# Kernel tuning notes

Hardware: AMD Instinct MI355X
Metric: run time of the kernel (lower is better)

The kernel has to match this reference:

```python
import jax, jax.numpy as jnp
import numpy as np

B, N, D_MODEL, H = 4, 2048, 1024, 16  # batch, seq, model dim, heads


def setup_inputs() -> dict:
    key = jax.random.key(0)
    k1, k2, k3 = jax.random.split(key, 3)
    x = jax.random.normal(k1, (B, N, D_MODEL), dtype=jnp.float32)
    # nn.Linear weights: [out_features, in_features]; scaled for stability
    Wqkv = jax.random.normal(k2, (3 * D_MODEL, D_MODEL), dtype=jnp.float32) * 0.02
    bqkv = jnp.zeros((3 * D_MODEL,), dtype=jnp.float32)
    Wo = jax.random.normal(k3, (D_MODEL, D_MODEL), dtype=jnp.float32) * 0.02
    bo = jnp.zeros((D_MODEL,), dtype=jnp.float32)
    return {"x": x, "Wqkv": Wqkv, "bqkv": bqkv, "Wo": Wo, "bo": bo}


def reference(x, Wqkv, bqkv, Wo, bo):
    b, n, _ = x.shape
    qkv = x @ Wqkv.T + bqkv                      # [b, n, 3*d_model]
    # rearrange 'b n (h d) -> b h n d' with h heads, then chunk into q,k,v
    qkv = qkv.reshape(b, n, H, -1).transpose(0, 2, 1, 3)  # [b, h, n, 3*dh]
    q, k, v = jnp.split(qkv, 3, axis=-1)          # each [b, h, n, dh]
    scale = k.shape[-1] ** 0.5
    scores = jnp.einsum('bhqd,bhkd->bhqk', q, k) / scale
    attn = jax.nn.softmax(scores, axis=-1)
    out = jnp.einsum('bhqk,bhkd->bhqd', attn, v)  # [b, h, n, dh]
    out = out.transpose(0, 2, 1, 3).reshape(b, n, -1)  # 'b h n d -> b n (h d)'
    return out @ Wo.T + bo
```

## Files before the change

### kernel.cpp

```cpp
#include <hip/hip_runtime.h>
#include <hip/hip_bf16.h>

using bf16 = __hip_bfloat16;
typedef __attribute__((ext_vector_type(8))) __bf16 bf16x8;
typedef __attribute__((ext_vector_type(4))) float f32x4;
typedef __attribute__((ext_vector_type(16))) float f32x16;
typedef __attribute__((ext_vector_type(4))) unsigned u32x4;

#define MFMA16(a, b, c) __builtin_amdgcn_mfma_f32_16x16x32_bf16((a), (b), (c), 0, 0, 0)
#define MFMA32(a, b, c) __builtin_amdgcn_mfma_f32_32x32x16_bf16((a), (b), (c), 0, 0, 0)

static __device__ __forceinline__ void gload_lds16(const bf16* g, bf16* l) {
    __builtin_amdgcn_global_load_lds(
        (__attribute__((address_space(1))) void*)(bf16*)(g),
        (__attribute__((address_space(3))) void*)(l), 16, 0, 0);
}

static __device__ __forceinline__ unsigned cvtpk(float lo, float hi) {
    unsigned r;
    asm("v_cvt_pk_bf16_f32 %0, %1, %2" : "=v"(r) : "v"(lo), "v"(hi));
    return r;
}

__global__ void cvt_f32_bf16(const float* __restrict__ in, bf16* __restrict__ out, int n4) {
    int i = blockIdx.x * 256 + threadIdx.x;
    if (i >= n4) return;
    float4 v = ((const float4*)in)[i];
    bf16 t[4];
    t[0] = __float2bfloat16(v.x);
    t[1] = __float2bfloat16(v.y);
    t[2] = __float2bfloat16(v.z);
    t[3] = __float2bfloat16(v.w);
    *(uint2*)(out + 4l * i) = *(uint2*)t;
}

__global__ void gemm_qkv(const bf16* __restrict__ A, const bf16* __restrict__ B,
                         const float* __restrict__ bias,
                         bf16* __restrict__ Qo, bf16* __restrict__ Ko, bf16* __restrict__ Vt) {
    const int K = 1024;
    __shared__ bf16 Alds[128 * 32];
    __shared__ bf16 Blds[128 * 32];
    int t = threadIdx.x;
    int lane = t & 63;
    int wave = t >> 6;
    int wm = wave >> 1, wn = wave & 1;
    int r = lane & 15, q = lane >> 4;
    long m0 = (long)blockIdx.y * 128;
    long n0 = (long)blockIdx.x * 128;
    const bf16* Ab = A + m0 * K;
    const bf16* Bb = B + n0 * K;

    f32x4 acc[4][4] = {};

    int srow = t >> 2;
    int scol = (t & 3) << 3;

    for (int k0 = 0; k0 < K; k0 += 32) {
        __syncthreads();
        gload_lds16(Ab + (long)srow * K + k0 + scol, Alds + t * 8);
        gload_lds16(Ab + (long)(srow + 64) * K + k0 + scol, Alds + 2048 + t * 8);
        gload_lds16(Bb + (long)srow * K + k0 + scol, Blds + t * 8);
        gload_lds16(Bb + (long)(srow + 64) * K + k0 + scol, Blds + 2048 + t * 8);
        __syncthreads();

        bf16x8 af[4], bfv[4];
#pragma unroll
        for (int mi = 0; mi < 4; mi++)
            af[mi] = *(const bf16x8*)(Alds + (wm * 64 + mi * 16 + r) * 32 + q * 8);
#pragma unroll
        for (int ni = 0; ni < 4; ni++)
            bfv[ni] = *(const bf16x8*)(Blds + (wn * 64 + ni * 16 + r) * 32 + q * 8);
#pragma unroll
        for (int mi = 0; mi < 4; mi++)
#pragma unroll
            for (int ni = 0; ni < 4; ni++)
                acc[mi][ni] = MFMA16(af[mi], bfv[ni], acc[mi][ni]);
    }

#pragma unroll
    for (int ni = 0; ni < 4; ni++) {
        int n = (int)n0 + wn * 64 + ni * 16 + r;
        float bn = bias[n];
        int h = n / 192;
        int rem = n % 192;
        int part = rem >> 6;
        int d = rem & 63;
#pragma unroll
        for (int mi = 0; mi < 4; mi++) {
#pragma unroll
            for (int rr = 0; rr < 4; rr++) {
                int m = (int)m0 + wm * 64 + mi * 16 + q * 4 + rr;
                int b = m >> 11;
                int row = m & 2047;
                long bh = b * 16 + h;
                bf16 bv = __float2bfloat16(acc[mi][ni][rr] + bn);
                if (part == 0)      Qo[(bh * 2048 + row) * 64 + d] = bv;
                else if (part == 1) Ko[(bh * 2048 + row) * 64 + d] = bv;
                else                Vt[(bh * 64 + d) * 2048 + row] = bv;
            }
        }
    }
}


#define PACK8(S, OFF, OUTV) { \
    unsigned A0 = cvtpk(S[OFF+0], S[OFF+1]); \
    unsigned B0 = cvtpk(S[OFF+4], S[OFF+5]); \
    unsigned A1 = cvtpk(S[OFF+2], S[OFF+3]); \
    unsigned B1 = cvtpk(S[OFF+6], S[OFF+7]); \
    asm("v_permlane32_swap_b32 %0, %1" : "+v"(A0), "+v"(B0)); \
    asm("v_permlane32_swap_b32 %0, %1" : "+v"(A1), "+v"(B1)); \
    u32x4 W; W.x = A0; W.y = A1; W.z = B0; W.w = B1; \
    OUTV = __builtin_bit_cast(bf16x8, W); }

#define COMPUTE(KB, VB) do { \
    f32x16 sA = {}, sB = {}; \
    __builtin_amdgcn_s_setprio(1); \
    { \
        bf16x8 kA, kB; \
        kA = *(const bf16x8*)(KB + (0 * 64 + lane) * 8); \
        kB = *(const bf16x8*)(KB + (256 + 0 * 64 + lane) * 8); \
        sA = MFMA32(kA, qf0, sA);  sB = MFMA32(kB, qf0, sB); \
        kA = *(const bf16x8*)(KB + (1 * 64 + lane) * 8); \
        kB = *(const bf16x8*)(KB + (256 + 1 * 64 + lane) * 8); \
        sA = MFMA32(kA, qf1, sA);  sB = MFMA32(kB, qf1, sB); \
        kA = *(const bf16x8*)(KB + (2 * 64 + lane) * 8); \
        kB = *(const bf16x8*)(KB + (256 + 2 * 64 + lane) * 8); \
        sA = MFMA32(kA, qf2, sA);  sB = MFMA32(kB, qf2, sB); \
        kA = *(const bf16x8*)(KB + (3 * 64 + lane) * 8); \
        kB = *(const bf16x8*)(KB + (256 + 3 * 64 + lane) * 8); \
        sA = MFMA32(kA, qf3, sA);  sB = MFMA32(kB, qf3, sB); \
    } \
    __builtin_amdgcn_s_setprio(0); \
    float x0 = fmaxf(fmaxf(sA[0], sA[1]), fmaxf(sA[2], sA[3])); \
    float x1 = fmaxf(fmaxf(sA[4], sA[5]), fmaxf(sA[6], sA[7])); \
    float x2 = fmaxf(fmaxf(sA[8], sA[9]), fmaxf(sA[10], sA[11])); \
    float x3 = fmaxf(fmaxf(sA[12], sA[13]), fmaxf(sA[14], sA[15])); \
    float y0 = fmaxf(fmaxf(sB[0], sB[1]), fmaxf(sB[2], sB[3])); \
    float y1 = fmaxf(fmaxf(sB[4], sB[5]), fmaxf(sB[6], sB[7])); \
    float y2 = fmaxf(fmaxf(sB[8], sB[9]), fmaxf(sB[10], sB[11])); \
    float y3 = fmaxf(fmaxf(sB[12], sB[13]), fmaxf(sB[14], sB[15])); \
    float pm = fmaxf(fmaxf(fmaxf(x0, x1), fmaxf(x2, x3)), \
                     fmaxf(fmaxf(y0, y1), fmaxf(y2, y3))); \
    pm = fmaxf(pm, __shfl_xor(pm, 32)); \
    bool resc = !__all(pm <= mv + 8.0f); \
    if (resc) { \
        float mn = fmaxf(mv, pm); \
        float al = __builtin_amdgcn_exp2f((mv - mn) * C1); \
        mv = mn; \
        lv *= al; \
        _Pragma("unroll") for (int e = 0; e < 16; ++e) { o0[e] *= al; o1[e] *= al; } \
    } \
    float mc = mv * C1; \
    float ts = 0.f; \
    _Pragma("unroll") for (int e = 0; e < 16; ++e) { float p = __builtin_amdgcn_exp2f(sA[e] * C1 - mc); sA[e] = p; ts += p; } \
    _Pragma("unroll") for (int e = 0; e < 16; ++e) { float p = __builtin_amdgcn_exp2f(sB[e] * C1 - mc); sB[e] = p; ts += p; } \
    ts += __shfl_xor(ts, 32); \
    lv += ts; \
    bf16x8 pf0, pf1, pf2, pf3; \
    PACK8(sA, 0, pf0); PACK8(sA, 8, pf1); PACK8(sB, 0, pf2); PACK8(sB, 8, pf3); \
    __builtin_amdgcn_s_setprio(1); \
    { \
        bf16x8 vA, vB; \
        vA = *(const bf16x8*)(VB + (0 * 64 + lane) * 8); \
        vB = *(const bf16x8*)(VB + (256 + 0 * 64 + lane) * 8); \
        o0 = MFMA32(vA, pf0, o0);  o1 = MFMA32(vB, pf0, o1); \
        vA = *(const bf16x8*)(VB + (1 * 64 + lane) * 8); \
        vB = *(const bf16x8*)(VB + (256 + 1 * 64 + lane) * 8); \
        o0 = MFMA32(vA, pf1, o0);  o1 = MFMA32(vB, pf1, o1); \
        vA = *(const bf16x8*)(VB + (2 * 64 + lane) * 8); \
        vB = *(const bf16x8*)(VB + (256 + 2 * 64 + lane) * 8); \
        o0 = MFMA32(vA, pf2, o0);  o1 = MFMA32(vB, pf2, o1); \
        vA = *(const bf16x8*)(VB + (3 * 64 + lane) * 8); \
        vB = *(const bf16x8*)(VB + (256 + 3 * 64 + lane) * 8); \
        o0 = MFMA32(vA, pf3, o0);  o1 = MFMA32(vB, pf3, o1); \
    } \
    __builtin_amdgcn_s_setprio(0); \
} while (0)

__global__ __launch_bounds__(512, 4) void attn_fwd(const bf16* __restrict__ Q,
                                                   const bf16* __restrict__ Kg,
                                                   const bf16* __restrict__ Vt,
                                                   bf16* __restrict__ AO) {
    __shared__ bf16 smem[16384];
    bf16* K0 = smem;
    bf16* V0 = smem + 4096;
    bf16* K1 = smem + 8192;
    bf16* V1 = smem + 12288;
    const int t = threadIdx.x;
    const int lane = t & 63, wave = t >> 6;
    const int l31 = lane & 31, hi = lane >> 5;
    const int bid = blockIdx.x;
    const int xcd = bid & 7, idx = bid >> 3;
    const int bh = xcd * 8 + (idx >> 3);
    const int qt = idx & 7;
    const float C1 = 0.18033688011112042f;

    bf16x8 qf0, qf1, qf2, qf3;
    {
        const bf16* Qb = Q + ((long)bh * 2048 + qt * 256 + wave * 32 + l31) * 64 + hi * 8;
        qf0 = *(const bf16x8*)(Qb + 0);
        qf1 = *(const bf16x8*)(Qb + 16);
        qf2 = *(const bf16x8*)(Qb + 32);
        qf3 = *(const bf16x8*)(Qb + 48);
    }

    const bf16* Kh = Kg + (long)bh * 2048 * 64;
    const bf16* Vh = Vt + (long)bh * 64 * 2048;

    const int sr = ((t >> 8) << 5) + (t & 31);
    const int sc = ((t >> 6) & 3) * 16 + ((t >> 5) & 1) * 8;

    f32x16 o0 = {}, o1 = {};
    float mv = -1e30f, lv = 0.f;

    auto issue_stage = [&](bf16* Kb, bf16* Vb, int kv0) {
        gload_lds16(Kh + (long)(kv0 + sr) * 64 + sc, Kb + t * 8);
        gload_lds16(Vh + (long)sr * 2048 + kv0 + sc, Vb + t * 8);
    };

    issue_stage(K0, V0, 0);
    __syncthreads();

    for (int kv0 = 0;; kv0 += 128) {
        issue_stage(K1, V1, kv0 + 64);
        COMPUTE(K0, V0);
        __syncthreads();
        if (kv0 + 128 < 2048) issue_stage(K0, V0, kv0 + 128);
        COMPUTE(K1, V1);
        if (kv0 + 128 >= 2048) break;
        __syncthreads();
    }

    long bb = bh >> 4, hh = bh & 15;
    __syncthreads();
    float il = 1.f / lv;
    char* wbase = (char*)smem + wave * 4096 + l31 * 128;
#pragma unroll
    for (int j = 0; j < 4; ++j) {
        unsigned wlo = cvtpk(o0[4 * j] * il, o0[4 * j + 1] * il);
        unsigned whi = cvtpk(o0[4 * j + 2] * il, o0[4 * j + 3] * il);
        int b8 = 2 * j + hi;
        int b8s = b8 ^ ((l31 & 7) << 1);
        uint2 val; val.x = wlo; val.y = whi;
        *(uint2*)(wbase + b8s * 8) = val;
    }
#pragma unroll
    for (int j = 0; j < 4; ++j) {
        unsigned wlo = cvtpk(o1[4 * j] * il, o1[4 * j + 1] * il);
        unsigned whi = cvtpk(o1[4 * j + 2] * il, o1[4 * j + 3] * il);
        int b8 = 8 + 2 * j + hi;
        int b8s = b8 ^ ((l31 & 7) << 1);
        uint2 val; val.x = wlo; val.y = whi;
        *(uint2*)(wbase + b8s * 8) = val;
    }
    __syncthreads();
    {
        int rid = t >> 1, hf = t & 1;
        int wv = rid >> 5, qq = rid & 31;
        long orow = (long)qt * 256 + wv * 32 + qq;
        const char* rbase = (const char*)smem + wv * 4096 + qq * 128;
        bf16* dst = AO + (bb * 2048 + orow) * 1024 + hh * 64 + hf * 32;
#pragma unroll
        for (int k = 0; k < 4; ++k) {
            int b8 = hf * 8 + 2 * k;
            int b8s = b8 ^ ((qq & 7) << 1);
            int4 v = *(const int4*)(rbase + b8s * 8);
            *(int4*)(dst + k * 8) = v;
        }
    }
}

__global__ void gemm_out(const bf16* __restrict__ A, const bf16* __restrict__ B,
                         const float* __restrict__ bias, float* __restrict__ C) {
    const int K = 1024, N = 1024;
    __shared__ bf16 Alds[128 * 32];
    __shared__ bf16 Blds[128 * 32];
    int t = threadIdx.x;
    int lane = t & 63;
    int wave = t >> 6;
    int wm = wave >> 1, wn = wave & 1;
    int r = lane & 15, q = lane >> 4;
    long m0 = (long)blockIdx.y * 128;
    long n0 = (long)blockIdx.x * 128;
    const bf16* Ab = A + m0 * K;
    const bf16* Bb = B + n0 * K;

    f32x4 acc[4][4] = {};

    int srow = t >> 2;
    int scol = (t & 3) << 3;

    for (int k0 = 0; k0 < K; k0 += 32) {
        __syncthreads();
        gload_lds16(Ab + (long)srow * K + k0 + scol, Alds + t * 8);
        gload_lds16(Ab + (long)(srow + 64) * K + k0 + scol, Alds + 2048 + t * 8);
        gload_lds16(Bb + (long)srow * K + k0 + scol, Blds + t * 8);
        gload_lds16(Bb + (long)(srow + 64) * K + k0 + scol, Blds + 2048 + t * 8);
        __syncthreads();

        bf16x8 af[4], bfv[4];
#pragma unroll
        for (int mi = 0; mi < 4; mi++)
            af[mi] = *(const bf16x8*)(Alds + (wm * 64 + mi * 16 + r) * 32 + q * 8);
#pragma unroll
        for (int ni = 0; ni < 4; ni++)
            bfv[ni] = *(const bf16x8*)(Blds + (wn * 64 + ni * 16 + r) * 32 + q * 8);
#pragma unroll
        for (int mi = 0; mi < 4; mi++)
#pragma unroll
            for (int ni = 0; ni < 4; ni++)
                acc[mi][ni] = MFMA16(af[mi], bfv[ni], acc[mi][ni]);
    }

#pragma unroll
    for (int ni = 0; ni < 4; ni++) {
        int n = (int)n0 + wn * 64 + ni * 16 + r;
        float bn = bias[n];
#pragma unroll
        for (int mi = 0; mi < 4; mi++) {
#pragma unroll
            for (int rr = 0; rr < 4; rr++) {
                long m = m0 + wm * 64 + mi * 16 + q * 4 + rr;
                C[m * N + n] = acc[mi][ni][rr] + bn;
            }
        }
    }
}

extern "C" void kernel_launch(void* const* d_in, const int* in_sizes, int n_in,
                              void* d_out, int out_size, void* d_ws, size_t ws_size,
                              hipStream_t stream) {
    const float* x    = (const float*)d_in[0];
    const float* Wqkv = (const float*)d_in[1];
    const float* bqkv = (const float*)d_in[2];
    const float* Wo   = (const float*)d_in[3];
    const float* bo   = (const float*)d_in[4];
    float* out = (float*)d_out;

    char* ws = (char*)d_ws;
    bf16* Xb  = (bf16*)(ws + 0);
    bf16* Wqb = (bf16*)(ws + 16777216);
    bf16* Wob = (bf16*)(ws + 23068672);
    bf16* Qb  = (bf16*)(ws + 25165824);
    bf16* Kb  = (bf16*)(ws + 41943040);
    bf16* Vtb = (bf16*)(ws + 58720256);
    bf16* AOb = (bf16*)(ws + 75497472);

    cvt_f32_bf16<<<8192, 256, 0, stream>>>(x, Xb, 8192 * 1024 / 4);
    cvt_f32_bf16<<<3072, 256, 0, stream>>>(Wqkv, Wqb, 3072 * 1024 / 4);
    cvt_f32_bf16<<<1024, 256, 0, stream>>>(Wo, Wob, 1024 * 1024 / 4);

    gemm_qkv<<<dim3(24, 64), 256, 0, stream>>>(Xb, Wqb, bqkv, Qb, Kb, Vtb);
    attn_fwd<<<512, 512, 0, stream>>>(Qb, Kb, Vtb, AOb);
    gemm_out<<<dim3(8, 64), 256, 0, stream>>>(AOb, Wob, bo, out);
}
```

Measured before the change: 205.5 us.

## Double-buffer GEMM LDS tiles, remap blocks per XCD, fuse conversion kernels

Both projection GEMMs now double-buffer their LDS tiles, so the next K-slice is loaded while MFMAs run on the current one, and each iteration needs one barrier instead of two. Blocks are remapped from a 1D grid so that neighbouring M tiles land on the same XCD, which should improve L2 reuse of the A and B panels. The three fp32-to-bf16 conversion launches are merged into a single kernel, and the softmax row-sum in attention becomes a vector add plus a tree reduction instead of a serial accumulation. Doubling LDS per block may lower occupancy.

```diff
diff --git a/kernel.cpp b/kernel.cpp
--- a/kernel.cpp
+++ b/kernel.cpp
@@ -22,31 +22,42 @@
     return r;
 }
 
-__global__ void cvt_f32_bf16(const float* __restrict__ in, bf16* __restrict__ out, int n4) {
-    int i = blockIdx.x * 256 + threadIdx.x;
-    if (i >= n4) return;
-    float4 v = ((const float4*)in)[i];
+__global__ void cvt_all(const float* __restrict__ x, const float* __restrict__ wq,
+                        const float* __restrict__ wo,
+                        bf16* __restrict__ xb, bf16* __restrict__ wqb, bf16* __restrict__ wob) {
+    int b = blockIdx.x;
+    const float* src;
+    bf16* dst;
+    long i;
+    if (b < 8192)       { src = x;  dst = xb;  i = (long)b * 256 + threadIdx.x; }
+    else if (b < 11264) { src = wq; dst = wqb; i = (long)(b - 8192) * 256 + threadIdx.x; }
+    else                { src = wo; dst = wob; i = (long)(b - 11264) * 256 + threadIdx.x; }
+    float4 v = ((const float4*)src)[i];
     bf16 t[4];
     t[0] = __float2bfloat16(v.x);
     t[1] = __float2bfloat16(v.y);
     t[2] = __float2bfloat16(v.z);
     t[3] = __float2bfloat16(v.w);
-    *(uint2*)(out + 4l * i) = *(uint2*)t;
+    *(uint2*)(dst + 4l * i) = *(uint2*)t;
 }
 
 __global__ void gemm_qkv(const bf16* __restrict__ A, const bf16* __restrict__ B,
                          const float* __restrict__ bias,
                          bf16* __restrict__ Qo, bf16* __restrict__ Ko, bf16* __restrict__ Vt) {
     const int K = 1024;
-    __shared__ bf16 Alds[128 * 32];
-    __shared__ bf16 Blds[128 * 32];
+    __shared__ bf16 Alds[2][4096];
+    __shared__ bf16 Blds[2][4096];
     int t = threadIdx.x;
     int lane = t & 63;
     int wave = t >> 6;
     int wm = wave >> 1, wn = wave & 1;
     int r = lane & 15, q = lane >> 4;
-    long m0 = (long)blockIdx.y * 128;
-    long n0 = (long)blockIdx.x * 128;
+    int lin = blockIdx.x;
+    int xcd = lin & 7, rr_ = lin >> 3;
+    int mi = xcd * 8 + rr_ / 24;
+    int ni = rr_ % 24;
+    long m0 = (long)mi * 128;
+    long n0 = (long)ni * 128;
     const bf16* Ab = A + m0 * K;
     const bf16* Bb = B + n0 * K;
 
@@ -55,45 +66,55 @@
     int srow = t >> 2;
     int scol = (t & 3) << 3;
 
-    for (int k0 = 0; k0 < K; k0 += 32) {
+    auto stage = [&](int buf, int k0) {
+        gload_lds16(Ab + (long)srow * K + k0 + scol, Alds[buf] + t * 8);
+        gload_lds16(Ab + (long)(srow + 64) * K + k0 + scol, Alds[buf] + 2048 + t * 8);
+        gload_lds16(Bb + (long)srow * K + k0 + scol, Blds[buf] + t * 8);
+        gload_lds16(Bb + (long)(srow + 64) * K + k0 + scol, Blds[buf] + 2048 + t * 8);
+    };
+    auto compute = [&](int buf) {
+        bf16x8 af[4], bfv[4];
+#pragma unroll
+        for (int mi4 = 0; mi4 < 4; mi4++)
+            af[mi4] = *(const bf16x8*)(Alds[buf] + (wm * 64 + mi4 * 16 + r) * 32 + q * 8);
+#pragma unroll
+        for (int ni4 = 0; ni4 < 4; ni4++)
+            bfv[ni4] = *(const bf16x8*)(Blds[buf] + (wn * 64 + ni4 * 16 + r) * 32 + q * 8);
+#pragma unroll
+        for (int mi4 = 0; mi4 < 4; mi4++)
+#pragma unroll
+            for (int ni4 = 0; ni4 < 4; ni4++)
+                acc[mi4][ni4] = MFMA16(af[mi4], bfv[ni4], acc[mi4][ni4]);
+    };
+
+    stage(0, 0);
+    __syncthreads();
+    int cur = 0;
+    for (int k0 = 32; k0 < K; k0 += 32) {
+        stage(cur ^ 1, k0);
+        compute(cur);
         __syncthreads();
-        gload_lds16(Ab + (long)srow * K + k0 + scol, Alds + t * 8);
-        gload_lds16(Ab + (long)(srow + 64) * K + k0 + scol, Alds + 2048 + t * 8);
-        gload_lds16(Bb + (long)srow * K + k0 + scol, Blds + t * 8);
-        gload_lds16(Bb + (long)(srow + 64) * K + k0 + scol, Blds + 2048 + t * 8);
-        __syncthreads();
-
-        bf16x8 af[4], bfv[4];
-#pragma unroll
-        for (int mi = 0; mi < 4; mi++)
-            af[mi] = *(const bf16x8*)(Alds + (wm * 64 + mi * 16 + r) * 32 + q * 8);
-#pragma unroll
-        for (int ni = 0; ni < 4; ni++)
-            bfv[ni] = *(const bf16x8*)(Blds + (wn * 64 + ni * 16 + r) * 32 + q * 8);
-#pragma unroll
-        for (int mi = 0; mi < 4; mi++)
-#pragma unroll
-            for (int ni = 0; ni < 4; ni++)
-                acc[mi][ni] = MFMA16(af[mi], bfv[ni], acc[mi][ni]);
-    }
-
-#pragma unroll
-    for (int ni = 0; ni < 4; ni++) {
-        int n = (int)n0 + wn * 64 + ni * 16 + r;
+        cur ^= 1;
+    }
+    compute(cur);
+
+#pragma unroll
+    for (int ni4 = 0; ni4 < 4; ni4++) {
+        int n = (int)n0 + wn * 64 + ni4 * 16 + r;
         float bn = bias[n];
         int h = n / 192;
         int rem = n % 192;
         int part = rem >> 6;
         int d = rem & 63;
 #pragma unroll
-        for (int mi = 0; mi < 4; mi++) {
+        for (int mi4 = 0; mi4 < 4; mi4++) {
 #pragma unroll
             for (int rr = 0; rr < 4; rr++) {
-                int m = (int)m0 + wm * 64 + mi * 16 + q * 4 + rr;
+                int m = (int)m0 + wm * 64 + mi4 * 16 + q * 4 + rr;
                 int b = m >> 11;
                 int row = m & 2047;
                 long bh = b * 16 + h;
-                bf16 bv = __float2bfloat16(acc[mi][ni][rr] + bn);
+                bf16 bv = __float2bfloat16(acc[mi4][ni4][rr] + bn);
                 if (part == 0)      Qo[(bh * 2048 + row) * 64 + d] = bv;
                 else if (part == 1) Ko[(bh * 2048 + row) * 64 + d] = bv;
                 else                Vt[(bh * 64 + d) * 2048 + row] = bv;
@@ -152,11 +173,18 @@
         _Pragma("unroll") for (int e = 0; e < 16; ++e) { o0[e] *= al; o1[e] *= al; } \
     } \
     float mc = mv * C1; \
-    float ts = 0.f; \
-    _Pragma("unroll") for (int e = 0; e < 16; ++e) { float p = __builtin_amdgcn_exp2f(sA[e] * C1 - mc); sA[e] = p; ts += p; } \
-    _Pragma("unroll") for (int e = 0; e < 16; ++e) { float p = __builtin_amdgcn_exp2f(sB[e] * C1 - mc); sB[e] = p; ts += p; } \
-    ts += __shfl_xor(ts, 32); \
-    lv += ts; \
+    _Pragma("unroll") for (int e = 0; e < 16; ++e) sA[e] = __builtin_amdgcn_exp2f(sA[e] * C1 - mc); \
+    _Pragma("unroll") for (int e = 0; e < 16; ++e) sB[e] = __builtin_amdgcn_exp2f(sB[e] * C1 - mc); \
+    { \
+        f32x16 scv = sA + sB; \
+        float u0 = (scv[0] + scv[1]) + (scv[2] + scv[3]); \
+        float u1 = (scv[4] + scv[5]) + (scv[6] + scv[7]); \
+        float u2 = (scv[8] + scv[9]) + (scv[10] + scv[11]); \
+        float u3 = (scv[12] + scv[13]) + (scv[14] + scv[15]); \
+        float ts = (u0 + u1) + (u2 + u3); \
+        ts += __shfl_xor(ts, 32); \
+        lv += ts; \
+    } \
     bf16x8 pf0, pf1, pf2, pf3; \
     PACK8(sA, 0, pf0); PACK8(sA, 8, pf1); PACK8(sB, 0, pf2); PACK8(sB, 8, pf3); \
     __builtin_amdgcn_s_setprio(1); \
@@ -274,15 +302,19 @@
 __global__ void gemm_out(const bf16* __restrict__ A, const bf16* __restrict__ B,
                          const float* __restrict__ bias, float* __restrict__ C) {
     const int K = 1024, N = 1024;
-    __shared__ bf16 Alds[128 * 32];
-    __shared__ bf16 Blds[128 * 32];
+    __shared__ bf16 Alds[2][4096];
+    __shared__ bf16 Blds[2][4096];
     int t = threadIdx.x;
     int lane = t & 63;
     int wave = t >> 6;
     int wm = wave >> 1, wn = wave & 1;
     int r = lane & 15, q = lane >> 4;
-    long m0 = (long)blockIdx.y * 128;
-    long n0 = (long)blockIdx.x * 128;
+    int lin = blockIdx.x;
+    int xcd = lin & 7, rr_ = lin >> 3;
+    int mi = xcd * 8 + (rr_ >> 3);
+    int ni = rr_ & 7;
+    long m0 = (long)mi * 128;
+    long n0 = (long)ni * 128;
     const bf16* Ab = A + m0 * K;
     const bf16* Bb = B + n0 * K;
 
@@ -291,38 +323,48 @@
     int srow = t >> 2;
     int scol = (t & 3) << 3;
 
-    for (int k0 = 0; k0 < K; k0 += 32) {
+    auto stage = [&](int buf, int k0) {
+        gload_lds16(Ab + (long)srow * K + k0 + scol, Alds[buf] + t * 8);
+        gload_lds16(Ab + (long)(srow + 64) * K + k0 + scol, Alds[buf] + 2048 + t * 8);
+        gload_lds16(Bb + (long)srow * K + k0 + scol, Blds[buf] + t * 8);
+        gload_lds16(Bb + (long)(srow + 64) * K + k0 + scol, Blds[buf] + 2048 + t * 8);
+    };
+    auto compute = [&](int buf) {
+        bf16x8 af[4], bfv[4];
+#pragma unroll
+        for (int mi4 = 0; mi4 < 4; mi4++)
+            af[mi4] = *(const bf16x8*)(Alds[buf] + (wm * 64 + mi4 * 16 + r) * 32 + q * 8);
+#pragma unroll
+        for (int ni4 = 0; ni4 < 4; ni4++)
+            bfv[ni4] = *(const bf16x8*)(Blds[buf] + (wn * 64 + ni4 * 16 + r) * 32 + q * 8);
+#pragma unroll
+        for (int mi4 = 0; mi4 < 4; mi4++)
+#pragma unroll
+            for (int ni4 = 0; ni4 < 4; ni4++)
+                acc[mi4][ni4] = MFMA16(af[mi4], bfv[ni4], acc[mi4][ni4]);
+    };
+
+    stage(0, 0);
+    __syncthreads();
+    int cur = 0;
+    for (int k0 = 32; k0 < K; k0 += 32) {
+        stage(cur ^ 1, k0);
+        compute(cur);
         __syncthreads();
-        gload_lds16(Ab + (long)srow * K + k0 + scol, Alds + t * 8);
-        gload_lds16(Ab + (long)(srow + 64) * K + k0 + scol, Alds + 2048 + t * 8);
-        gload_lds16(Bb + (long)srow * K + k0 + scol, Blds + t * 8);
-        gload_lds16(Bb + (long)(srow + 64) * K + k0 + scol, Blds + 2048 + t * 8);
-        __syncthreads();
-
-        bf16x8 af[4], bfv[4];
-#pragma unroll
-        for (int mi = 0; mi < 4; mi++)
-            af[mi] = *(const bf16x8*)(Alds + (wm * 64 + mi * 16 + r) * 32 + q * 8);
-#pragma unroll
-        for (int ni = 0; ni < 4; ni++)
-            bfv[ni] = *(const bf16x8*)(Blds + (wn * 64 + ni * 16 + r) * 32 + q * 8);
-#pragma unroll
-        for (int mi = 0; mi < 4; mi++)
-#pragma unroll
-            for (int ni = 0; ni < 4; ni++)
-                acc[mi][ni] = MFMA16(af[mi], bfv[ni], acc[mi][ni]);
-    }
-
-#pragma unroll
-    for (int ni = 0; ni < 4; ni++) {
-        int n = (int)n0 + wn * 64 + ni * 16 + r;
+        cur ^= 1;
+    }
+    compute(cur);
+
+#pragma unroll
+    for (int ni4 = 0; ni4 < 4; ni4++) {
+        int n = (int)n0 + wn * 64 + ni4 * 16 + r;
         float bn = bias[n];
 #pragma unroll
-        for (int mi = 0; mi < 4; mi++) {
+        for (int mi4 = 0; mi4 < 4; mi4++) {
 #pragma unroll
             for (int rr = 0; rr < 4; rr++) {
-                long m = m0 + wm * 64 + mi * 16 + q * 4 + rr;
-                C[m * N + n] = acc[mi][ni][rr] + bn;
+                long m = m0 + wm * 64 + mi4 * 16 + q * 4 + rr;
+                C[m * N + n] = acc[mi4][ni4][rr] + bn;
             }
         }
     }
@@ -347,11 +389,9 @@
     bf16* Vtb = (bf16*)(ws + 58720256);
     bf16* AOb = (bf16*)(ws + 75497472);
 
-    cvt_f32_bf16<<<8192, 256, 0, stream>>>(x, Xb, 8192 * 1024 / 4);
-    cvt_f32_bf16<<<3072, 256, 0, stream>>>(Wqkv, Wqb, 3072 * 1024 / 4);
-    cvt_f32_bf16<<<1024, 256, 0, stream>>>(Wo, Wob, 1024 * 1024 / 4);
-
-    gemm_qkv<<<dim3(24, 64), 256, 0, stream>>>(Xb, Wqb, bqkv, Qb, Kb, Vtb);
+    cvt_all<<<12288, 256, 0, stream>>>(x, Wqkv, Wo, Xb, Wqb, Wob);
+
+    gemm_qkv<<<1536, 256, 0, stream>>>(Xb, Wqb, bqkv, Qb, Kb, Vtb);
     attn_fwd<<<512, 512, 0, stream>>>(Qb, Kb, Vtb, AOb);
-    gemm_out<<<dim3(8, 64), 256, 0, stream>>>(AOb, Wob, bo, out);
-}
+    gemm_out<<<512, 256, 0, stream>>>(AOb, Wob, bo, out);
+}
```

Result: faster. 201.3 us (-2.0%).
